# Performance work log

Hardware: AMD Instinct MI355X
Metric: run time of the kernel (lower is better)

Reference implementation:

```python
import jax, jax.numpy as jnp
import numpy as np

B, T, D, H, E, K = 8, 1024, 384, 6, 4, 1
HS = D // H          # 64
FF = 4 * D           # 1536
EPS = 1e-5


def setup_inputs() -> dict:
    key = jax.random.key(0)
    ks = jax.random.split(key, 16)
    s = lambda k, shape, fan: jax.random.normal(k, shape, jnp.float32) * (fan ** -0.5)
    return {
        "x": jax.random.normal(ks[0], (B, T, D), jnp.float32),
        "ln1_g": jnp.ones((D,), jnp.float32), "ln1_b": jnp.zeros((D,), jnp.float32),
        "Wq": s(ks[1], (H, D, HS), D), "Wk": s(ks[2], (H, D, HS), D), "Wv": s(ks[3], (H, D, HS), D),
        "Wo": s(ks[4], (D, D), D), "bo": jnp.zeros((D,), jnp.float32),
        "ln2_g": jnp.ones((D,), jnp.float32), "ln2_b": jnp.zeros((D,), jnp.float32),
        "Wg": s(ks[5], (D, E), D),
        "W1": s(ks[6], (E, D, FF), D), "b1": jnp.zeros((E, FF), jnp.float32),
        "W2": s(ks[7], (E, FF, D), FF), "b2": jnp.zeros((E, D), jnp.float32),
    }


def _ln(x, g, b):
    m = jnp.mean(x, -1, keepdims=True)
    v = jnp.mean((x - m) ** 2, -1, keepdims=True)
    return (x - m) * jax.lax.rsqrt(v + EPS) * g + b


def reference(x, ln1_g, ln1_b, Wq, Wk, Wv, Wo, bo, ln2_g, ln2_b, Wg, W1, b1, W2, b2):
    # --- multi-head causal attention (note: scale uses n_embed, as in source) ---
    h = _ln(x, ln1_g, ln1_b)                      # [B,T,D]
    q = jnp.einsum('btd,hde->bhte', h, Wq)
    k = jnp.einsum('btd,hde->bhte', h, Wk)
    v = jnp.einsum('btd,hde->bhte', h, Wv)
    wei = jnp.einsum('bhte,bhse->bhts', q, k) * (D ** -0.5)
    causal = jnp.tril(jnp.ones((T, T), bool))
    wei = jnp.where(causal, wei, -jnp.inf)
    wei = jax.nn.softmax(wei, axis=-1)
    att = jnp.einsum('bhts,bhse->bhte', wei, v)   # [B,H,T,HS]
    att = att.transpose(0, 2, 1, 3).reshape(B, T, D)
    x = x + att @ Wo + bo

    # --- MoE FFN, top-k routing (k=1) ---
    h2 = _ln(x, ln2_g, ln2_b).reshape(-1, D)      # [N,D]
    logits = h2 @ Wg                              # [N,E]
    w, sel = jax.lax.top_k(logits, K)             # [N,K]
    w = jax.nn.softmax(w.astype(jnp.float32), axis=1).astype(h2.dtype)
    combine = (jax.nn.one_hot(sel, E, dtype=h2.dtype) * w[..., None]).sum(1)  # [N,E]
    eh = jax.nn.relu(jnp.einsum('nd,edf->enf', h2, W1) + b1[:, None, :])       # [E,N,FF]
    eo = jnp.einsum('enf,efd->end', eh, W2) + b2[:, None, :]                   # [E,N,D]
    moe = jnp.einsum('ne,end->nd', combine, eo)
    return x + moe.reshape(B, T, D)
```

## Files before the change

### kernel.cpp

```cpp
#include <hip/hip_runtime.h>
#include <math.h>

#define NEG_INF (-1e30f)
#define INV_SQRT_D 0.051031036f
#define RLO (1.0f/2048.0f)
#define RP  (1.0f/16384.0f)

typedef short bfrag  __attribute__((ext_vector_type(8)));
typedef _Float16 h8  __attribute__((ext_vector_type(8)));
typedef float f32x4  __attribute__((ext_vector_type(4)));

__device__ __forceinline__ float4 ld4(const float* p) { return *(const float4*)p; }
__device__ __forceinline__ ushort f2bf(float x) {
  unsigned u = __float_as_uint(x);
  return (ushort)((u + 0x7fffu + ((u >> 16) & 1u)) >> 16);
}
__device__ __forceinline__ void split2h(float v, ushort& hi, ushort& lo) {
  _Float16 h = (_Float16)v;
  _Float16 l = (_Float16)((v - (float)h) * 2048.0f);
  hi = __builtin_bit_cast(ushort, h);
  lo = __builtin_bit_cast(ushort, l);
}

#define MFMA16(a, b, c) __builtin_amdgcn_mfma_f32_16x16x32_f16((a), (b), (c), 0, 0, 0)

__global__ __launch_bounds__(256) void ln1_split(const float* __restrict__ x,
    const float* __restrict__ g, const float* __restrict__ b,
    ushort* __restrict__ hh, ushort* __restrict__ hl) {
  int lane = threadIdx.x & 63;
  int n = blockIdx.x * 4 + (threadIdx.x >> 6);
  const float* xp = x + (size_t)n * 384;
  float v[6]; float s = 0.f;
#pragma unroll
  for (int i = 0; i < 6; i++) { v[i] = xp[lane + 64*i]; s += v[i]; }
#pragma unroll
  for (int o = 32; o; o >>= 1) s += __shfl_xor(s, o);
  float m = s / 384.0f;
  float vs = 0.f;
#pragma unroll
  for (int i = 0; i < 6; i++) { float d = v[i] - m; vs += d * d; }
#pragma unroll
  for (int o = 32; o; o >>= 1) vs += __shfl_xor(vs, o);
  float rs = 1.0f / sqrtf(vs / 384.0f + 1e-5f);
#pragma unroll
  for (int i = 0; i < 6; i++) {
    int d = lane + 64*i;
    float hv = (v[i] - m) * rs * g[d] + b[d];
    ushort hi, lo; split2h(hv, hi, lo);
    hh[(size_t)n * 384 + d] = hi;
    hl[(size_t)n * 384 + d] = lo;
  }
}

__global__ __launch_bounds__(256) void wsplitT(const float* __restrict__ in,
    ushort* __restrict__ oh, ushort* __restrict__ ol, int C, int in_zstride) {
  __shared__ float ts[32][33];
  int z = blockIdx.z;
  int c0 = blockIdx.x * 32, r0 = blockIdx.y * 32;
  const float* ip = in + (size_t)z * in_zstride;
  int t = threadIdx.x;
  int ir = t >> 3, ic = (t & 7) * 4;
  float4 v = ld4(ip + (size_t)(r0 + ir) * C + c0 + ic);
  ts[ir][ic] = v.x; ts[ir][ic+1] = v.y; ts[ir][ic+2] = v.z; ts[ir][ic+3] = v.w;
  __syncthreads();
  ushort4 vh, vl;
  ushort h_, l_;
  split2h(ts[ic+0][ir], h_, l_); vh.x = h_; vl.x = l_;
  split2h(ts[ic+1][ir], h_, l_); vh.y = h_; vl.y = l_;
  split2h(ts[ic+2][ir], h_, l_); vh.z = h_; vl.z = l_;
  split2h(ts[ic+3][ir], h_, l_); vh.w = h_; vl.w = l_;
  size_t idx = ((size_t)(z * C + c0 + ir)) * 384 + r0 + ic;
  *(ushort4*)(oh + idx) = vh;
  *(ushort4*)(ol + idx) = vl;
}

template<int MODE>
__global__ __launch_bounds__(256) void mm_split(
    const ushort* __restrict__ Ah, const ushort* __restrict__ Al,
    const ushort* __restrict__ Bh, const ushort* __restrict__ Bl,
    ushort* __restrict__ o1h, ushort* __restrict__ o1l,
    ushort* __restrict__ o2h, ushort* __restrict__ o2l,
    const float* __restrict__ bias, const float* __restrict__ xres,
    float* __restrict__ outf) {
  __shared__ alignas(16) ushort Ash[128][40], Asl[128][40], Bsh[128][40], Bsl[128][40];
  int tid = threadIdx.x;
  int bx = blockIdx.x, by = blockIdx.y;
  int r0 = by * 128, n0 = bx * 128;
  int lane = tid & 63, wv = tid >> 6;
  int wr = (wv >> 1) * 64, wc = (wv & 1) * 64;
  int srow = tid >> 1, sseg = tid & 1;
  int cc = lane & 15, cg = lane >> 4;

  const ushort* arh = Ah + (size_t)(r0 + srow) * 384 + sseg * 16;
  const ushort* arl = Al + (size_t)(r0 + srow) * 384 + sseg * 16;
  const ushort* brh = Bh + (size_t)(n0 + srow) * 384 + sseg * 16;
  const ushort* brl = Bl + (size_t)(n0 + srow) * 384 + sseg * 16;

  f32x4 ach[4][4], acc[4][4];
#pragma unroll
  for (int m = 0; m < 4; m++)
#pragma unroll
    for (int n = 0; n < 4; n++) {
      ach[m][n] = (f32x4){0.f, 0.f, 0.f, 0.f};
      acc[m][n] = (f32x4){0.f, 0.f, 0.f, 0.f};
    }

  for (int kt = 0; kt < 12; kt++) {
    int kc = kt * 32;
    float4 ah0 = ld4((const float*)(arh + kc));
    float4 ah1 = ld4((const float*)(arh + kc + 8));
    float4 al0 = ld4((const float*)(arl + kc));
    float4 al1 = ld4((const float*)(arl + kc + 8));
    float4 bh0 = ld4((const float*)(brh + kc));
    float4 bh1 = ld4((const float*)(brh + kc + 8));
    float4 bl0 = ld4((const float*)(brl + kc));
    float4 bl1 = ld4((const float*)(brl + kc + 8));
    __syncthreads();
    *(float4*)&Ash[srow][sseg*16]   = ah0; *(float4*)&Ash[srow][sseg*16+8] = ah1;
    *(float4*)&Asl[srow][sseg*16]   = al0; *(float4*)&Asl[srow][sseg*16+8] = al1;
    *(float4*)&Bsh[srow][sseg*16]   = bh0; *(float4*)&Bsh[srow][sseg*16+8] = bh1;
    *(float4*)&Bsl[srow][sseg*16]   = bl0; *(float4*)&Bsl[srow][sseg*16+8] = bl1;
    __syncthreads();
#pragma unroll
    for (int m = 0; m < 4; m++) {
      h8 afh = *(const h8*)&Ash[wr + m*16 + cc][cg*8];
      h8 afl = *(const h8*)&Asl[wr + m*16 + cc][cg*8];
#pragma unroll
      for (int n = 0; n < 4; n++) {
        h8 bfh = *(const h8*)&Bsh[wc + n*16 + cc][cg*8];
        h8 bfl = *(const h8*)&Bsl[wc + n*16 + cc][cg*8];
        ach[m][n] = MFMA16(afh, bfh, ach[m][n]);
        acc[m][n] = MFMA16(afh, bfl, acc[m][n]);
        acc[m][n] = MFMA16(afl, bfh, acc[m][n]);
      }
    }
  }

  int cr = cg * 4;
  if constexpr (MODE == 0) {
    int matq = bx / 3;
    ushort* oh = matq ? o2h : o1h;
    ushort* ol = matq ? o2l : o1l;
#pragma unroll
    for (int m = 0; m < 4; m++)
#pragma unroll
      for (int n = 0; n < 4; n++)
#pragma unroll
        for (int r_ = 0; r_ < 4; r_++) {
          int colg = n0 + wc + n*16 + cc;
          int head = (colg >> 6) % 6;
          int e = colg & 63;
          int rowg = r0 + wr + m*16 + cr + r_;
          int b = rowg >> 10, t = rowg & 1023;
          size_t idx = ((size_t)(b*6 + head) * 1024 + t) * 64 + e;
          float val = ach[m][n][r_] + acc[m][n][r_] * RLO;
          ushort hi, lo; split2h(val, hi, lo);
          oh[idx] = hi; ol[idx] = lo;
        }
  } else if constexpr (MODE == 1) {
#pragma unroll
    for (int m = 0; m < 4; m++)
#pragma unroll
      for (int n = 0; n < 4; n++)
#pragma unroll
        for (int r_ = 0; r_ < 4; r_++) {
          int rowg = r0 + wr + m*16 + cr + r_;
          int h = rowg >> 6, e = rowg & 63;
          int colg = n0 + wc + n*16 + cc;
          int b = colg >> 10, t = colg & 1023;
          size_t idx = ((size_t)(b*6 + h) * 64 + e) * 1024 + t;
          float val = ach[m][n][r_] + acc[m][n][r_] * RLO;
          ushort hi, lo; split2h(val, hi, lo);
          o1h[idx] = hi; o1l[idx] = lo;
        }
  } else {
#pragma unroll
    for (int m = 0; m < 4; m++)
#pragma unroll
      for (int n = 0; n < 4; n++)
#pragma unroll
        for (int r_ = 0; r_ < 4; r_++) {
          int rowg = r0 + wr + m*16 + cr + r_;
          int colg = n0 + wc + n*16 + cc;
          size_t idx = (size_t)rowg * 384 + colg;
          outf[idx] = xres[idx] + bias[colg] + (ach[m][n][r_] + acc[m][n][r_] * RLO);
        }
  }
}

__global__ __launch_bounds__(256) void attn_mfma(
    const ushort* __restrict__ qh, const ushort* __restrict__ ql,
    const ushort* __restrict__ kh, const ushort* __restrict__ kl,
    const ushort* __restrict__ vth, const ushort* __restrict__ vtl,
    ushort* __restrict__ atth, ushort* __restrict__ attl) {
  __shared__ alignas(16) ushort Qh[64][72], Ql[64][72], Kh[64][72], Kl[64][72],
                                Vh[64][72], Vl[64][72], Ph[64][72], Pl[64][72];
  int bh = blockIdx.x;
  int qt = 15 - blockIdx.y;
  int tid = threadIdx.x, lane = tid & 63, wv = tid >> 6;
  int cc = lane & 15, cg = lane >> 4;
  int row = tid >> 2, seg = (tid & 3) * 16;

  {
    const ushort* s0 = qh + ((size_t)bh * 1024 + qt * 64 + row) * 64 + seg;
    const ushort* s1 = ql + ((size_t)bh * 1024 + qt * 64 + row) * 64 + seg;
    *(float4*)&Qh[row][seg]   = ld4((const float*)s0);
    *(float4*)&Qh[row][seg+8] = ld4((const float*)(s0 + 8));
    *(float4*)&Ql[row][seg]   = ld4((const float*)s1);
    *(float4*)&Ql[row][seg+8] = ld4((const float*)(s1 + 8));
  }

  float m_[4], l_[4];
  f32x4 aOh[4], aOc[4];
#pragma unroll
  for (int r = 0; r < 4; r++) { m_[r] = NEG_INF; l_[r] = 0.f; }
#pragma unroll
  for (int n = 0; n < 4; n++) {
    aOh[n] = (f32x4){0.f, 0.f, 0.f, 0.f};
    aOc[n] = (f32x4){0.f, 0.f, 0.f, 0.f};
  }

  for (int st = 0; st <= qt; st++) {
    {
      const ushort* s0 = kh + ((size_t)bh * 1024 + st * 64 + row) * 64 + seg;
      const ushort* s1 = kl + ((size_t)bh * 1024 + st * 64 + row) * 64 + seg;
      const ushort* s2 = vth + ((size_t)bh * 64 + row) * 1024 + st * 64 + seg;
      const ushort* s3 = vtl + ((size_t)bh * 64 + row) * 1024 + st * 64 + seg;
      *(float4*)&Kh[row][seg]   = ld4((const float*)s0);
      *(float4*)&Kh[row][seg+8] = ld4((const float*)(s0 + 8));
      *(float4*)&Kl[row][seg]   = ld4((const float*)s1);
      *(float4*)&Kl[row][seg+8] = ld4((const float*)(s1 + 8));
      *(float4*)&Vh[row][seg]   = ld4((const float*)s2);
      *(float4*)&Vh[row][seg+8] = ld4((const float*)(s2 + 8));
      *(float4*)&Vl[row][seg]   = ld4((const float*)s3);
      *(float4*)&Vl[row][seg+8] = ld4((const float*)(s3 + 8));
    }
    __syncthreads();

    f32x4 aSh[4], aSc[4];
#pragma unroll
    for (int n = 0; n < 4; n++) {
      aSh[n] = (f32x4){0.f, 0.f, 0.f, 0.f};
      aSc[n] = (f32x4){0.f, 0.f, 0.f, 0.f};
    }
#pragma unroll
    for (int kk = 0; kk < 2; kk++) {
      h8 aqh = *(const h8*)&Qh[wv*16 + cc][cg*8 + kk*32];
      h8 aql = *(const h8*)&Ql[wv*16 + cc][cg*8 + kk*32];
#pragma unroll
      for (int n = 0; n < 4; n++) {
        h8 bkh = *(const h8*)&Kh[n*16 + cc][cg*8 + kk*32];
        h8 bkl = *(const h8*)&Kl[n*16 + cc][cg*8 + kk*32];
        aSh[n] = MFMA16(aqh, bkh, aSh[n]);
        aSc[n] = MFMA16(aqh, bkl, aSc[n]);
        aSc[n] = MFMA16(aql, bkh, aSc[n]);
      }
    }

#pragma unroll
    for (int r = 0; r < 4; r++) {
      int t_loc = wv*16 + cg*4 + r;
      int t_glob = qt*64 + t_loc;
      float sv[4]; float rmax = NEG_INF;
#pragma unroll
      for (int n = 0; n < 4; n++) {
        float s_ = (aSh[n][r] + aSc[n][r] * RLO) * INV_SQRT_D;
        int s_glob = st*64 + n*16 + cc;
        if (st == qt && s_glob > t_glob) s_ = NEG_INF;
        sv[n] = s_;
        rmax = fmaxf(rmax, s_);
      }
#pragma unroll
      for (int o = 8; o; o >>= 1) rmax = fmaxf(rmax, __shfl_xor(rmax, o));
      float mn = fmaxf(m_[r], rmax);
      float sc = expf(m_[r] - mn);
      m_[r] = mn;
      float rsum = 0.f;
#pragma unroll
      for (int n = 0; n < 4; n++) { float p = expf(sv[n] - mn); sv[n] = p; rsum += p; }
#pragma unroll
      for (int o = 8; o; o >>= 1) rsum += __shfl_xor(rsum, o);
      l_[r] = l_[r] * sc + rsum;
#pragma unroll
      for (int n = 0; n < 4; n++) {
        aOh[n][r] *= sc;
        aOc[n][r] *= sc;
        ushort hi, lo; split2h(sv[n] * 16384.0f, hi, lo);
        Ph[t_loc][n*16 + cc] = hi;
        Pl[t_loc][n*16 + cc] = lo;
      }
    }

#pragma unroll
    for (int kk = 0; kk < 2; kk++) {
      h8 pah = *(const h8*)&Ph[wv*16 + cc][cg*8 + kk*32];
      h8 pal = *(const h8*)&Pl[wv*16 + cc][cg*8 + kk*32];
#pragma unroll
      for (int n = 0; n < 4; n++) {
        h8 bvh = *(const h8*)&Vh[n*16 + cc][cg*8 + kk*32];
        h8 bvl = *(const h8*)&Vl[n*16 + cc][cg*8 + kk*32];
        aOh[n] = MFMA16(pah, bvh, aOh[n]);
        aOc[n] = MFMA16(pah, bvl, aOc[n]);
        aOc[n] = MFMA16(pal, bvh, aOc[n]);
      }
    }
    __syncthreads();
  }

  int b_ = bh / 6, h_ = bh % 6;
#pragma unroll
  for (int n = 0; n < 4; n++)
#pragma unroll
    for (int r = 0; r < 4; r++) {
      int t_loc = wv*16 + cg*4 + r;
      float val = (aOh[n][r] + aOc[n][r] * RLO) * RP / l_[r];
      size_t idx = ((size_t)b_ * 1024 + qt*64 + t_loc) * 384 + h_*64 + n*16 + cc;
      ushort hi, lo; split2h(val, hi, lo);
      atth[idx] = hi; attl[idx] = lo;
    }
}

__global__ __launch_bounds__(256) void ln2gate_kernel(const float* __restrict__ x1,
    const float* __restrict__ g, const float* __restrict__ b, const float* __restrict__ Wg,
    ushort* __restrict__ h2, int* __restrict__ meta) {
  int lane = threadIdx.x & 63;
  int n = blockIdx.x * 4 + (threadIdx.x >> 6);
  const float* xp = x1 + (size_t)n * 384;
  float v[6]; float s = 0.f;
#pragma unroll
  for (int i = 0; i < 6; i++) { v[i] = xp[lane + 64*i]; s += v[i]; }
#pragma unroll
  for (int o = 32; o; o >>= 1) s += __shfl_xor(s, o);
  float m = s / 384.0f;
  float vs = 0.f;
#pragma unroll
  for (int i = 0; i < 6; i++) { float d = v[i] - m; vs += d * d; }
#pragma unroll
  for (int o = 32; o; o >>= 1) vs += __shfl_xor(vs, o);
  float rs = 1.0f / sqrtf(vs / 384.0f + 1e-5f);
  float4 ag = make_float4(0.f, 0.f, 0.f, 0.f);
#pragma unroll
  for (int i = 0; i < 6; i++) {
    int d = lane + 64*i;
    float hv = (v[i] - m) * rs * g[d] + b[d];
    h2[(size_t)n * 384 + d] = f2bf(hv);
    float4 w = ld4(Wg + d * 4);
    ag.x = fmaf(hv, w.x, ag.x); ag.y = fmaf(hv, w.y, ag.y);
    ag.z = fmaf(hv, w.z, ag.z); ag.w = fmaf(hv, w.w, ag.w);
  }
#pragma unroll
  for (int o = 32; o; o >>= 1) {
    ag.x += __shfl_xor(ag.x, o); ag.y += __shfl_xor(ag.y, o);
    ag.z += __shfl_xor(ag.z, o); ag.w += __shfl_xor(ag.w, o);
  }
  if (lane == 0) {
    int best = 0; float bv = ag.x;
    if (ag.y > bv) { bv = ag.y; best = 1; }
    if (ag.z > bv) { bv = ag.z; best = 2; }
    if (ag.w > bv) { bv = ag.w; best = 3; }
    meta[16 + 8704 + n] = best;
  }
}

__global__ __launch_bounds__(1024) void hist_kernel(int* __restrict__ meta) {
  const int* sel = meta + 16 + 8704;
  int tid = threadIdx.x;
  int c[4] = {0, 0, 0, 0};
#pragma unroll
  for (int i = 0; i < 8; i++) {
    int e = sel[tid + 1024 * i];
#pragma unroll
    for (int x = 0; x < 4; x++) c[x] += (e == x);
  }
#pragma unroll
  for (int x = 0; x < 4; x++)
#pragma unroll
    for (int o = 32; o; o >>= 1) c[x] += __shfl_xor(c[x], o);
  __shared__ int wsum[16][4];
  int lane = tid & 63, wv = tid >> 6;
  if (lane == 0) {
#pragma unroll
    for (int x = 0; x < 4; x++) wsum[wv][x] = c[x];
  }
  __syncthreads();
  if (tid == 0) {
    int tot[4] = {0, 0, 0, 0};
    for (int w = 0; w < 16; w++)
#pragma unroll
      for (int x = 0; x < 4; x++) tot[x] += wsum[w][x];
    int off = 0;
#pragma unroll
    for (int x = 0; x < 4; x++) {
      meta[x] = tot[x];
      meta[4 + x] = 0;
      meta[8 + x] = off;
      off += (tot[x] + 127) & ~127;
    }
    meta[12] = off;
  }
}

__global__ __launch_bounds__(256) void scatter_kernel(int* __restrict__ meta) {
  int n = blockIdx.x * 256 + threadIdx.x;
  int lane = threadIdx.x & 63;
  int e = meta[16 + 8704 + n];
#pragma unroll
  for (int x = 0; x < 4; x++) {
    unsigned long long mask = __ballot(e == x);
    if (mask == 0ull) continue;
    int leader = __ffsll((unsigned long long)mask) - 1;
    int cnt = __popcll(mask);
    int base = 0;
    if (lane == leader) base = atomicAdd(meta + 4 + x, cnt);
    base = __shfl(base, leader);
    if (e == x) {
      int rank = __popcll(mask & ((1ull << lane) - 1ull));
      meta[16 + meta[8 + x] + base + rank] = n;
    }
  }
}

__global__ __launch_bounds__(256) void wtrans(const float* __restrict__ in,
    ushort* __restrict__ out, int R, int C) {
  __shared__ float ts[32][33];
  int mat = blockIdx.z;
  int c0 = blockIdx.x * 32, r0 = blockIdx.y * 32;
  const float* ip = in + (size_t)mat * R * C;
  ushort* op = out + (size_t)mat * R * C;
  int t = threadIdx.x;
  int ir = t >> 3, ic = (t & 7) * 4;
  float4 v = ld4(ip + (size_t)(r0 + ir) * C + c0 + ic);
  ts[ir][ic] = v.x; ts[ir][ic + 1] = v.y; ts[ir][ic + 2] = v.z; ts[ir][ic + 3] = v.w;
  __syncthreads();
  ushort4 o;
  o.x = f2bf(ts[ic + 0][ir]); o.y = f2bf(ts[ic + 1][ir]);
  o.z = f2bf(ts[ic + 2][ir]); o.w = f2bf(ts[ic + 3][ir]);
  *(ushort4*)(op + (size_t)(c0 + ir) * R + r0 + ic) = o;
}

template<int MODE>
__global__ __launch_bounds__(256) void moe_mfma(
    const ushort* __restrict__ Abf, const ushort* __restrict__ Bbf,
    const float* __restrict__ bias, float* __restrict__ outf,
    ushort* __restrict__ Ybf, const int* __restrict__ meta) {
  constexpr int K = MODE ? 1536 : 384;
  constexpr int N = MODE ? 384 : 1536;
  constexpr int NK = K / 32;
  __shared__ alignas(16) ushort As[128][40];
  __shared__ alignas(16) ushort Bs[128][40];
  int tid = threadIdx.x;
  int r0 = blockIdx.y * 128, n0 = blockIdx.x * 128;
  if (r0 >= meta[12]) return;
  int e = 0;
  if (r0 >= meta[9])  e = 1;
  if (r0 >= meta[10]) e = 2;
  if (r0 >= meta[11]) e = 3;
  const int* perm = meta + 16;
  const ushort* Bp = Bbf + (size_t)e * K * N;
  int lane = tid & 63, wv = tid >> 6;
  int wr = (wv >> 1) * 64, wc = (wv & 1) * 64;
  int srow = tid >> 1, sseg = tid & 1;

  const ushort* arow;
  if constexpr (MODE == 0) {
    int src = perm[r0 + srow];
    arow = (src >= 0) ? (Abf + (size_t)src * 384) : nullptr;
  } else {
    arow = Abf + (size_t)(r0 + srow) * 1536;
  }
  const ushort* brow = Bp + (size_t)(n0 + srow) * K;

  const bfrag* pa[4]; const bfrag* pb[4];
#pragma unroll
  for (int m = 0; m < 4; m++)
    pa[m] = (const bfrag*)&As[wr + m * 16 + (lane & 15)][(lane >> 4) * 8];
#pragma unroll
  for (int n = 0; n < 4; n++)
    pb[n] = (const bfrag*)&Bs[wc + n * 16 + (lane & 15)][(lane >> 4) * 8];

  f32x4 acc[4][4];
#pragma unroll
  for (int m = 0; m < 4; m++)
#pragma unroll
    for (int n = 0; n < 4; n++) acc[m][n] = (f32x4){0.f, 0.f, 0.f, 0.f};

  for (int kt = 0; kt < NK; kt++) {
    int kc = kt * 32;
    float4 av0, av1;
    if (arow) {
      av0 = ld4((const float*)(arow + kc + sseg * 16));
      av1 = ld4((const float*)(arow + kc + sseg * 16 + 8));
    } else {
      av0 = make_float4(0.f, 0.f, 0.f, 0.f); av1 = av0;
    }
    float4 bv0 = ld4((const float*)(brow + kc + sseg * 16));
    float4 bv1 = ld4((const float*)(brow + kc + sseg * 16 + 8));
    __syncthreads();
    *(float4*)&As[srow][sseg * 16] = av0;
    *(float4*)&As[srow][sseg * 16 + 8] = av1;
    *(float4*)&Bs[srow][sseg * 16] = bv0;
    *(float4*)&Bs[srow][sseg * 16 + 8] = bv1;
    __syncthreads();
    bfrag af[4], bfv[4];
#pragma unroll
    for (int m = 0; m < 4; m++) af[m] = *pa[m];
#pragma unroll
    for (int n = 0; n < 4; n++) bfv[n] = *pb[n];
#pragma unroll
    for (int m = 0; m < 4; m++)
#pragma unroll
      for (int n = 0; n < 4; n++)
        acc[m][n] = __builtin_amdgcn_mfma_f32_16x16x32_bf16(af[m], bfv[n], acc[m][n], 0, 0, 0);
  }

  int cr = (lane >> 4) * 4;
  int cc = lane & 15;
  if constexpr (MODE == 0) {
#pragma unroll
    for (int n = 0; n < 4; n++) {
      int col = n0 + wc + n * 16 + cc;
      float bv = bias[e * N + col];
#pragma unroll
      for (int m = 0; m < 4; m++) {
        int row = r0 + wr + m * 16 + cr;
#pragma unroll
        for (int r = 0; r < 4; r++) {
          float val = acc[m][n][r] + bv;
          val = fmaxf(val, 0.f);
          Ybf[(size_t)(row + r) * 1536 + col] = f2bf(val);
        }
      }
    }
  } else {
#pragma unroll
    for (int m = 0; m < 4; m++) {
      int rowb = r0 + wr + m * 16 + cr;
#pragma unroll
      for (int r = 0; r < 4; r++) {
        int tok = perm[rowb + r];
        if (tok < 0) continue;
#pragma unroll
        for (int n = 0; n < 4; n++) {
          int col = n0 + wc + n * 16 + cc;
          float* dst = outf + (size_t)tok * 384 + col;
          *dst = *dst + acc[m][n][r] + bias[e * N + col];
        }
      }
    }
  }
}

extern "C" void kernel_launch(void* const* d_in, const int* in_sizes, int n_in,
                              void* d_out, int out_size, void* d_ws, size_t ws_size,
                              hipStream_t stream) {
  const float* x    = (const float*)d_in[0];
  const float* ln1g = (const float*)d_in[1];
  const float* ln1b = (const float*)d_in[2];
  const float* Wq   = (const float*)d_in[3];
  const float* Wk   = (const float*)d_in[4];
  const float* Wv   = (const float*)d_in[5];
  const float* Wo   = (const float*)d_in[6];
  const float* bo   = (const float*)d_in[7];
  const float* ln2g = (const float*)d_in[8];
  const float* ln2b = (const float*)d_in[9];
  const float* Wg   = (const float*)d_in[10];
  const float* W1   = (const float*)d_in[11];
  const float* b1   = (const float*)d_in[12];
  const float* W2   = (const float*)d_in[13];
  const float* b2   = (const float*)d_in[14];
  float* out = (float*)d_out;
  float* ws  = (float*)d_ws;

  ushort* hhi    = (ushort*)ws;
  ushort* hlo    = (ushort*)(ws + 1572864);
  ushort* WqkvTh = (ushort*)(ws + 3145728);
  ushort* WqkvTl = (ushort*)(ws + 3366912);
  ushort* WoTh   = (ushort*)(ws + 3588096);
  ushort* WoTl   = (ushort*)(ws + 3661824);
  ushort* qhi    = (ushort*)(ws + 3735552);
  ushort* qlo    = (ushort*)(ws + 5308416);
  ushort* khi    = (ushort*)(ws + 6881280);
  ushort* klo    = (ushort*)(ws + 8454144);
  ushort* vthi   = (ushort*)(ws + 10027008);
  ushort* vtlo   = (ushort*)(ws + 11599872);
  ushort* atth   = (ushort*)(ws + 13172736);
  ushort* attl   = (ushort*)(ws + 14745600);
  int*    meta   = (int*)(ws + 16318464);
  ushort* h2b = (ushort*)ws;
  ushort* W1t = (ushort*)(ws + 3735552);
  ushort* W2t = (ushort*)(ws + 5308416);
  ushort* Y   = (ushort*)(ws + 6881280);

  hipMemsetAsync(meta + 16, 0xFF, 8704 * sizeof(int), stream);

  ln1_split<<<2048, 256, 0, stream>>>(x, ln1g, ln1b, hhi, hlo);
  wsplitT<<<dim3(2, 12, 6), 256, 0, stream>>>(Wq, WqkvTh,          WqkvTl,          64, 384*64);
  wsplitT<<<dim3(2, 12, 6), 256, 0, stream>>>(Wk, WqkvTh + 147456, WqkvTl + 147456, 64, 384*64);
  wsplitT<<<dim3(2, 12, 6), 256, 0, stream>>>(Wv, WqkvTh + 294912, WqkvTl + 294912, 64, 384*64);
  wsplitT<<<dim3(12, 12, 1), 256, 0, stream>>>(Wo, WoTh, WoTl, 384, 0);

  mm_split<0><<<dim3(6, 64), 256, 0, stream>>>(hhi, hlo, WqkvTh, WqkvTl,
      qhi, qlo, khi, klo, nullptr, nullptr, nullptr);
  mm_split<1><<<dim3(64, 3), 256, 0, stream>>>(WqkvTh + 294912, WqkvTl + 294912, hhi, hlo,
      vthi, vtlo, nullptr, nullptr, nullptr, nullptr, nullptr);
  attn_mfma<<<dim3(48, 16), 256, 0, stream>>>(qhi, qlo, khi, klo, vthi, vtlo, atth, attl);
  wtrans<<<dim3(48, 12, 4), 256, 0, stream>>>(W1, W1t, 384, 1536);
  wtrans<<<dim3(12, 48, 4), 256, 0, stream>>>(W2, W2t, 1536, 384);
  mm_split<2><<<dim3(3, 64), 256, 0, stream>>>(atth, attl, WoTh, WoTl,
      nullptr, nullptr, nullptr, nullptr, bo, x, out);
  ln2gate_kernel<<<2048, 256, 0, stream>>>(out, ln2g, ln2b, Wg, h2b, meta);
  hist_kernel<<<1, 1024, 0, stream>>>(meta);
  scatter_kernel<<<32, 256, 0, stream>>>(meta);
  moe_mfma<0><<<dim3(12, 68), 256, 0, stream>>>(h2b, W1t, b1, nullptr, Y, meta);
  moe_mfma<1><<<dim3(3, 68), 256, 0, stream>>>(Y, W2t, b2, out, nullptr, meta);
}
```

Measured before the change: 384.9 us.

## Keep Q in registers, fold softmax scale into Q projection, pack P hi/lo

The attention scale is now applied in the QKV projection epilogue instead of inside the attention inner loop. Q fragments are loaded straight from global memory into registers instead of being staged through shared memory. P hi/lo halves are packed into one 32-bit shared array and split again with byte permutes. The change also switches to fast __expf and raises wave priority around the MFMA blocks, trading some exp precision and extra permute instructions for less LDS traffic and footprint.

```diff
diff --git a/kernel.cpp b/kernel.cpp
--- a/kernel.cpp
+++ b/kernel.cpp
@@ -141,6 +141,7 @@
     int matq = bx / 3;
     ushort* oh = matq ? o2h : o1h;
     ushort* ol = matq ? o2l : o1l;
+    float scl = matq ? 1.0f : INV_SQRT_D;
 #pragma unroll
     for (int m = 0; m < 4; m++)
 #pragma unroll
@@ -153,7 +154,7 @@
           int rowg = r0 + wr + m*16 + cr + r_;
           int b = rowg >> 10, t = rowg & 1023;
           size_t idx = ((size_t)(b*6 + head) * 1024 + t) * 64 + e;
-          float val = ach[m][n][r_] + acc[m][n][r_] * RLO;
+          float val = (ach[m][n][r_] + acc[m][n][r_] * RLO) * scl;
           ushort hi, lo; split2h(val, hi, lo);
           oh[idx] = hi; ol[idx] = lo;
         }
@@ -193,21 +194,20 @@
     const ushort* __restrict__ kh, const ushort* __restrict__ kl,
     const ushort* __restrict__ vth, const ushort* __restrict__ vtl,
     ushort* __restrict__ atth, ushort* __restrict__ attl) {
-  __shared__ alignas(16) ushort Qh[64][72], Ql[64][72], Kh[64][72], Kl[64][72],
-                                Vh[64][72], Vl[64][72], Ph[64][72], Pl[64][72];
+  __shared__ alignas(16) ushort Kh[64][72], Kl[64][72], Vh[64][72], Vl[64][72];
+  __shared__ alignas(16) unsigned int Pp[64][68];
   int bh = blockIdx.x;
   int qt = 15 - blockIdx.y;
   int tid = threadIdx.x, lane = tid & 63, wv = tid >> 6;
   int cc = lane & 15, cg = lane >> 4;
   int row = tid >> 2, seg = (tid & 3) * 16;
 
+  h8 aq_h[2], aq_l[2];
   {
-    const ushort* s0 = qh + ((size_t)bh * 1024 + qt * 64 + row) * 64 + seg;
-    const ushort* s1 = ql + ((size_t)bh * 1024 + qt * 64 + row) * 64 + seg;
-    *(float4*)&Qh[row][seg]   = ld4((const float*)s0);
-    *(float4*)&Qh[row][seg+8] = ld4((const float*)(s0 + 8));
-    *(float4*)&Ql[row][seg]   = ld4((const float*)s1);
-    *(float4*)&Ql[row][seg+8] = ld4((const float*)(s1 + 8));
+    const ushort* qb = qh + ((size_t)bh * 1024 + qt * 64 + wv * 16 + cc) * 64 + cg * 8;
+    const ushort* qlb = ql + ((size_t)bh * 1024 + qt * 64 + wv * 16 + cc) * 64 + cg * 8;
+    aq_h[0] = *(const h8*)qb;       aq_h[1] = *(const h8*)(qb + 32);
+    aq_l[0] = *(const h8*)qlb;      aq_l[1] = *(const h8*)(qlb + 32);
   }
 
   float m_[4], l_[4];
@@ -243,19 +243,19 @@
       aSh[n] = (f32x4){0.f, 0.f, 0.f, 0.f};
       aSc[n] = (f32x4){0.f, 0.f, 0.f, 0.f};
     }
+    __builtin_amdgcn_s_setprio(1);
 #pragma unroll
     for (int kk = 0; kk < 2; kk++) {
-      h8 aqh = *(const h8*)&Qh[wv*16 + cc][cg*8 + kk*32];
-      h8 aql = *(const h8*)&Ql[wv*16 + cc][cg*8 + kk*32];
 #pragma unroll
       for (int n = 0; n < 4; n++) {
         h8 bkh = *(const h8*)&Kh[n*16 + cc][cg*8 + kk*32];
         h8 bkl = *(const h8*)&Kl[n*16 + cc][cg*8 + kk*32];
-        aSh[n] = MFMA16(aqh, bkh, aSh[n]);
-        aSc[n] = MFMA16(aqh, bkl, aSc[n]);
-        aSc[n] = MFMA16(aql, bkh, aSc[n]);
+        aSh[n] = MFMA16(aq_h[kk], bkh, aSh[n]);
+        aSc[n] = MFMA16(aq_h[kk], bkl, aSc[n]);
+        aSc[n] = MFMA16(aq_l[kk], bkh, aSc[n]);
       }
     }
+    __builtin_amdgcn_s_setprio(0);
 
 #pragma unroll
     for (int r = 0; r < 4; r++) {
@@ -264,7 +264,7 @@
       float sv[4]; float rmax = NEG_INF;
 #pragma unroll
       for (int n = 0; n < 4; n++) {
-        float s_ = (aSh[n][r] + aSc[n][r] * RLO) * INV_SQRT_D;
+        float s_ = aSh[n][r] + aSc[n][r] * RLO;
         int s_glob = st*64 + n*16 + cc;
         if (st == qt && s_glob > t_glob) s_ = NEG_INF;
         sv[n] = s_;
@@ -273,11 +273,11 @@
 #pragma unroll
       for (int o = 8; o; o >>= 1) rmax = fmaxf(rmax, __shfl_xor(rmax, o));
       float mn = fmaxf(m_[r], rmax);
-      float sc = expf(m_[r] - mn);
+      float sc = __expf(m_[r] - mn);
       m_[r] = mn;
       float rsum = 0.f;
 #pragma unroll
-      for (int n = 0; n < 4; n++) { float p = expf(sv[n] - mn); sv[n] = p; rsum += p; }
+      for (int n = 0; n < 4; n++) { float p = __expf(sv[n] - mn); sv[n] = p; rsum += p; }
 #pragma unroll
       for (int o = 8; o; o >>= 1) rsum += __shfl_xor(rsum, o);
       l_[r] = l_[r] * sc + rsum;
@@ -286,15 +286,25 @@
         aOh[n][r] *= sc;
         aOc[n][r] *= sc;
         ushort hi, lo; split2h(sv[n] * 16384.0f, hi, lo);
-        Ph[t_loc][n*16 + cc] = hi;
-        Pl[t_loc][n*16 + cc] = lo;
+        Pp[t_loc][n*16 + cc] = (unsigned int)hi | ((unsigned int)lo << 16);
       }
     }
 
 #pragma unroll
     for (int kk = 0; kk < 2; kk++) {
-      h8 pah = *(const h8*)&Ph[wv*16 + cc][cg*8 + kk*32];
-      h8 pal = *(const h8*)&Pl[wv*16 + cc][cg*8 + kk*32];
+      uint4 v0 = *(const uint4*)&Pp[wv*16 + cc][cg*8 + kk*32];
+      uint4 v1 = *(const uint4*)&Pp[wv*16 + cc][cg*8 + kk*32 + 4];
+      union { unsigned int u[4]; h8 h; } HH, LL;
+      HH.u[0] = __builtin_amdgcn_perm(v0.y, v0.x, 0x05040100u);
+      HH.u[1] = __builtin_amdgcn_perm(v0.w, v0.z, 0x05040100u);
+      HH.u[2] = __builtin_amdgcn_perm(v1.y, v1.x, 0x05040100u);
+      HH.u[3] = __builtin_amdgcn_perm(v1.w, v1.z, 0x05040100u);
+      LL.u[0] = __builtin_amdgcn_perm(v0.y, v0.x, 0x07060302u);
+      LL.u[1] = __builtin_amdgcn_perm(v0.w, v0.z, 0x07060302u);
+      LL.u[2] = __builtin_amdgcn_perm(v1.y, v1.x, 0x07060302u);
+      LL.u[3] = __builtin_amdgcn_perm(v1.w, v1.z, 0x07060302u);
+      h8 pah = HH.h, pal = LL.h;
+      __builtin_amdgcn_s_setprio(1);
 #pragma unroll
       for (int n = 0; n < 4; n++) {
         h8 bvh = *(const h8*)&Vh[n*16 + cc][cg*8 + kk*32];
@@ -303,6 +313,7 @@
         aOc[n] = MFMA16(pah, bvl, aOc[n]);
         aOc[n] = MFMA16(pal, bvh, aOc[n]);
       }
+      __builtin_amdgcn_s_setprio(0);
     }
     __syncthreads();
   }
```

Measured after the change: 364.7 us. 1.06x faster.
